# Performance work log

Hardware: AMD Instinct MI355X
Metric: run time of the kernel (lower is better)

## Reference

```python
import jax, jax.numpy as jnp
import numpy as np

N = 100000        # nodes
E = 1600000       # edges (avg degree 16)
IN = 128          # in_channels
HID = 256         # hidden_channels
OUT = 2           # out_channels
G = 512           # num graphs in batch


def setup_inputs() -> dict:
    key = jax.random.key(0)
    ks = jax.random.split(key, 10)
    x = jax.random.normal(ks[0], (N, IN), dtype=jnp.float32)
    edge_index = jax.random.randint(ks[1], (2, E), 0, N, dtype=jnp.int64)
    # sorted graph assignment, every graph non-empty (PyG-style batching)
    batch = (jnp.arange(N, dtype=jnp.int64) * G) // N
    s = 1.0 / np.sqrt(IN)
    sh = 1.0 / np.sqrt(2 * HID)
    sh1 = 1.0 / np.sqrt(HID)
    W_l = jax.random.uniform(ks[2], (HID, IN), jnp.float32, -s, s)   # SAGE lin_l (neighbors)
    b_l = jax.random.uniform(ks[3], (HID,), jnp.float32, -s, s)
    W_r = jax.random.uniform(ks[4], (HID, IN), jnp.float32, -s, s)   # SAGE lin_r (root), no bias
    W0 = jax.random.uniform(ks[5], (HID, IN), jnp.float32, -s, s)    # lin0
    b0 = jax.random.uniform(ks[5], (HID,), jnp.float32, -s, s)
    W1 = jax.random.uniform(ks[6], (HID, 2 * HID), jnp.float32, -sh, sh)  # lin1
    b1 = jax.random.uniform(ks[7], (HID,), jnp.float32, -sh, sh)
    W2 = jax.random.uniform(ks[8], (OUT, HID), jnp.float32, -sh1, sh1)    # lin2
    b2 = jax.random.uniform(ks[9], (OUT,), jnp.float32, -sh1, sh1)
    return {"x": x, "edge_index": edge_index, "batch": batch,
            "W_l": W_l, "b_l": b_l, "W_r": W_r,
            "W0": W0, "b0": b0, "W1": W1, "b1": b1, "W2": W2, "b2": b2}


def reference(x, edge_index, batch, W_l, b_l, W_r, W0, b0, W1, b1, W2, b2):
    src, dst = edge_index[0], edge_index[1]
    # SAGEConv: mean-aggregate neighbor features (gather -> scatter-add -> normalize)
    msg_sum = jax.ops.segment_sum(x[src], dst, num_segments=N)          # [N, IN]
    deg = jax.ops.segment_sum(jnp.ones((E,), x.dtype), dst, num_segments=N)
    aggr = msg_sum / jnp.maximum(deg, 1.0)[:, None]
    h = jax.nn.relu(aggr @ W_l.T + b_l + x @ W_r.T)                     # [N, HID]
    # global max pool per graph
    hp = jax.ops.segment_max(h, batch, num_segments=G)                  # [G, HID]
    # root node = first node of each graph (batch is sorted)
    root = jnp.searchsorted(batch, jnp.arange(G, dtype=batch.dtype))    # [G]
    news = jax.nn.relu(x[root] @ W0.T + b0)                             # [G, HID]
    h = jax.nn.relu(jnp.concatenate([news, hp], axis=-1) @ W1.T + b1)   # [G, HID]
    h = h @ W2.T + b2                                                   # [G, OUT]
    return jax.nn.log_softmax(h, axis=-1)
```

## Files before the change

kernel.cpp:

```cpp
#include <hip/hip_runtime.h>
#include <hip/hip_bf16.h>
#include <math.h>
#include <stdint.h>

#define IN_C 128
#define HID  256
#define OUT_C 2

#define BSHIFT 9
#define BNODES 512
#define EPB 4096

typedef __attribute__((ext_vector_type(8))) short short8;
typedef __attribute__((ext_vector_type(4))) float f32x4;
typedef __attribute__((ext_vector_type(2))) float f32x2;

#if defined(__has_builtin)
#if __has_builtin(__builtin_amdgcn_cvt_pk_f32_fp8) && __has_builtin(__builtin_amdgcn_cvt_pk_fp8_f32)
#define HAVE_FP8_CVT 1
#endif
#if __has_builtin(__builtin_amdgcn_global_load_lds)
#define HAVE_GLL 1
#endif
#endif

__device__ __forceinline__ ushort f2bf(float f) {
  uint32_t u = __float_as_uint(f);
  uint32_t r = u + 0x7FFF + ((u >> 16) & 1);
  return (ushort)(r >> 16);
}
__device__ __forceinline__ float bf2f(ushort b) {
  return __uint_as_float(((uint32_t)b) << 16);
}

#ifndef HAVE_FP8_CVT
__device__ __forceinline__ uint32_t f2fp8_1(float f) {
  uint32_t u = __float_as_uint(f);
  uint32_t s = (u >> 24) & 0x80;
  float a = fabsf(f);
  if (a >= 448.f) return s | 0x7E;
  if (a < 0.015625f) {
    uint32_t m = (uint32_t)(a * 512.f + 0.5f);
    return s | m;
  }
  uint32_t r = u & 0x7fffffff;
  r += 0x7FFFF + ((r >> 20) & 1);
  uint32_t e = (r >> 23) - 127;
  if ((int)e > 8) return s | 0x7E;
  return s | ((e + 7) << 3) | ((r >> 20) & 7);
}
__device__ __forceinline__ float fp8_2f(uint32_t b) {
  uint32_t s = (b & 0x80) << 24;
  uint32_t e = (b >> 3) & 0xF, m = b & 7;
  if (e == 0) { float f = (float)m * 0.001953125f; return s ? -f : f; }
  return __uint_as_float(s | ((e + 120) << 23) | (m << 20));
}
#endif

__device__ __forceinline__ void acc8f8(float* s, uint2 v) {
#ifdef HAVE_FP8_CVT
  f32x2 a = __builtin_amdgcn_cvt_pk_f32_fp8(v.x, false);
  f32x2 b = __builtin_amdgcn_cvt_pk_f32_fp8(v.x, true);
  f32x2 c = __builtin_amdgcn_cvt_pk_f32_fp8(v.y, false);
  f32x2 d = __builtin_amdgcn_cvt_pk_f32_fp8(v.y, true);
  s[0] += a.x; s[1] += a.y; s[2] += b.x; s[3] += b.y;
  s[4] += c.x; s[5] += c.y; s[6] += d.x; s[7] += d.y;
#else
  s[0] += fp8_2f(v.x & 0xff);        s[1] += fp8_2f((v.x >> 8) & 0xff);
  s[2] += fp8_2f((v.x >> 16) & 0xff); s[3] += fp8_2f(v.x >> 24);
  s[4] += fp8_2f(v.y & 0xff);        s[5] += fp8_2f((v.y >> 8) & 0xff);
  s[6] += fp8_2f((v.y >> 16) & 0xff); s[7] += fp8_2f(v.y >> 24);
#endif
}


__global__ void k_hist(const int* __restrict__ dst, int* __restrict__ bcount, int E) {
  __shared__ int h[256];
  int t = threadIdx.x;
  h[t] = 0;
  __syncthreads();
  for (int e = blockIdx.x * 256 + t; e < E; e += gridDim.x * 256)
    atomicAdd(&h[dst[e] >> BSHIFT], 1);
  __syncthreads();
  if (h[t]) atomicAdd(&bcount[t], h[t]);
}

__global__ void k_bucket_scan(const int* __restrict__ bcount,
                              int* __restrict__ bbase, int* __restrict__ bcursor) {
  __shared__ int sd[256];
  int t = threadIdx.x;
  int cnt = bcount[t];
  sd[t] = cnt;
  __syncthreads();
  for (int off = 1; off < 256; off <<= 1) {
    int v = (t >= off) ? sd[t - off] : 0;
    __syncthreads();
    sd[t] += v;
    __syncthreads();
  }
  int base = sd[t] - cnt;
  bbase[t] = base;
  bcursor[t] = base;
}

__global__ __launch_bounds__(256) void k_scatter(
    const int* __restrict__ src, const int* __restrict__ dst,
    int* __restrict__ bcursor, uint32_t* __restrict__ rec, int E) {
  __shared__ int h[256];
  __shared__ int bbase[256];
  __shared__ int lcur[256];
  int t = threadIdx.x;
  int e0 = blockIdx.x * EPB;
  int e1 = e0 + EPB < E ? e0 + EPB : E;
  h[t] = 0; lcur[t] = 0;
  __syncthreads();
  for (int e = e0 + t; e < e1; e += 256)
    atomicAdd(&h[dst[e] >> BSHIFT], 1);
  __syncthreads();
  if (h[t]) bbase[t] = atomicAdd(&bcursor[t], h[t]);
  __syncthreads();
  for (int e = e0 + t; e < e1; e += 256) {
    int d = dst[e];
    int b = d >> BSHIFT;
    int r = atomicAdd(&lcur[b], 1);
    rec[bbase[b] + r] = ((uint32_t)src[e] << BSHIFT) | ((uint32_t)d & (BNODES - 1));
  }
}

__global__ __launch_bounds__(256) void k_csr(
    const uint32_t* __restrict__ rec, const int* __restrict__ bbase,
    const int* __restrict__ bcount,
    int* __restrict__ row_start, int* __restrict__ deg,
    int* __restrict__ csr, int n) {
  __shared__ int ldeg[BNODES];
  __shared__ int lexcl[BNODES];
  __shared__ int ssum[256];
  int t = threadIdx.x;
  int b = blockIdx.x;
  int node0 = b << BSHIFT;
  int ebase = bbase[b];
  int ecnt = bcount[b];

  ldeg[t] = 0; ldeg[t + 256] = 0;
  __syncthreads();
  for (int i = t; i < ecnt; i += 256)
    atomicAdd(&ldeg[rec[ebase + i] & (BNODES - 1)], 1);
  __syncthreads();

  int v0 = ldeg[2 * t], v1 = ldeg[2 * t + 1];
  ssum[t] = v0 + v1;
  __syncthreads();
  for (int off = 1; off < 256; off <<= 1) {
    int v = (t >= off) ? ssum[t - off] : 0;
    __syncthreads();
    ssum[t] += v;
    __syncthreads();
  }
  int excl = ssum[t] - (v0 + v1);
  lexcl[2 * t] = excl;
  lexcl[2 * t + 1] = excl + v0;
  int node = node0 + 2 * t;
  if (node < n) { row_start[node] = ebase + excl; deg[node] = v0; }
  if (node + 1 < n) { row_start[node + 1] = ebase + excl + v0; deg[node + 1] = v1; }
  ldeg[2 * t] = 0; ldeg[2 * t + 1] = 0;
  __syncthreads();
  for (int i = t; i < ecnt; i += 256) {
    uint32_t r = rec[ebase + i];
    int li = r & (BNODES - 1);
    int k = atomicAdd(&ldeg[li], 1);
    csr[ebase + lexcl[li] + k] = (int)(r >> BSHIFT);
  }
}


__global__ void k_cast(const float* __restrict__ in, ushort* __restrict__ outb,
                       uint32_t* __restrict__ outf8, int n4) {
  int i = blockIdx.x * 256 + threadIdx.x;
  if (i < n4) {
    float4 v = ((const float4*)in)[i];
    ushort4 o;
    o.x = f2bf(v.x); o.y = f2bf(v.y); o.z = f2bf(v.z); o.w = f2bf(v.w);
    ((ushort4*)outb)[i] = o;
#ifdef HAVE_FP8_CVT
    int p = __builtin_amdgcn_cvt_pk_fp8_f32(v.x, v.y, 0, false);
    p = __builtin_amdgcn_cvt_pk_fp8_f32(v.z, v.w, p, true);
    outf8[i] = (uint32_t)p;
#else
    outf8[i] = f2fp8_1(v.x) | (f2fp8_1(v.y) << 8) | (f2fp8_1(v.z) << 16) |
               (f2fp8_1(v.w) << 24);
#endif
  }
}

__global__ void k_wcat(const float* __restrict__ Wl, const float* __restrict__ Wr,
                       ushort* __restrict__ Wcat) {
  int c = blockIdx.x, k = threadIdx.x;
  float v = (k < IN_C) ? Wl[(size_t)c * IN_C + k] : Wr[(size_t)c * IN_C + (k - IN_C)];
  Wcat[(size_t)c * (2 * IN_C) + k] = f2bf(v);
}

__global__ void k_cast2(const float* __restrict__ W0, const float* __restrict__ W1,
                        ushort* __restrict__ W0b, ushort* __restrict__ W1b) {
  const int N0 = HID * IN_C / 4;
  const int N1 = HID * 2 * HID / 4;
  int i = blockIdx.x * 256 + threadIdx.x;
  if (i < N0) {
    float4 v = ((const float4*)W0)[i];
    ushort4 o = {f2bf(v.x), f2bf(v.y), f2bf(v.z), f2bf(v.w)};
    ((ushort4*)W0b)[i] = o;
  } else if (i < N0 + N1) {
    int j = i - N0;
    float4 v = ((const float4*)W1)[j];
    ushort4 o = {f2bf(v.x), f2bf(v.y), f2bf(v.z), f2bf(v.w)};
    ((ushort4*)W1b)[j] = o;
  }
}


__global__ void k_aggr(const uint32_t* __restrict__ xf8, const int* __restrict__ csr,
                       const int* __restrict__ row_start, const int* __restrict__ deg,
                       ushort* __restrict__ aggr, int n) {
  int wid = threadIdx.x >> 6;
  int lane = threadIdx.x & 63;
  int node = blockIdx.x * 4 + wid;
  if (node >= n) return;
  int base = row_start[node];
  int d = deg[node];
  int q = lane >> 4, li = lane & 15;
  float s[8] = {};
  int i = q;
  for (; i + 12 < d; i += 16) {
    int n0 = csr[base + i];
    int n1 = csr[base + i + 4];
    int n2 = csr[base + i + 8];
    int n3 = csr[base + i + 12];
    uint2 a = ((const uint2*)(xf8 + (size_t)n0 * (IN_C / 4)))[li];
    uint2 b = ((const uint2*)(xf8 + (size_t)n1 * (IN_C / 4)))[li];
    uint2 c = ((const uint2*)(xf8 + (size_t)n2 * (IN_C / 4)))[li];
    uint2 e = ((const uint2*)(xf8 + (size_t)n3 * (IN_C / 4)))[li];
    acc8f8(s, a); acc8f8(s, b); acc8f8(s, c); acc8f8(s, e);
  }
  for (; i < d; i += 4) {
    int n0 = csr[base + i];
    uint2 a = ((const uint2*)(xf8 + (size_t)n0 * (IN_C / 4)))[li];
    acc8f8(s, a);
  }
#pragma unroll
  for (int j = 0; j < 8; ++j) {
    s[j] += __shfl_xor(s[j], 16);
    s[j] += __shfl_xor(s[j], 32);
  }
  if (q == 0) {
    float inv = 1.0f / (float)(d > 1 ? d : 1);
    uint4 o;
    o.x = (uint32_t)f2bf(s[0] * inv) | ((uint32_t)f2bf(s[1] * inv) << 16);
    o.y = (uint32_t)f2bf(s[2] * inv) | ((uint32_t)f2bf(s[3] * inv) << 16);
    o.z = (uint32_t)f2bf(s[4] * inv) | ((uint32_t)f2bf(s[5] * inv) << 16);
    o.w = (uint32_t)f2bf(s[6] * inv) | ((uint32_t)f2bf(s[7] * inv) << 16);
    ((uint4*)(aggr + (size_t)node * IN_C))[li] = o;
  }
}


#ifdef HAVE_GLL
__device__ __forceinline__ void load16_lds(const ushort* g, ushort* l) {
  __builtin_amdgcn_global_load_lds(
      (const __attribute__((address_space(1))) uint32_t*)g,
      (__attribute__((address_space(3))) uint32_t*)l, 16, 0, 0);
}
#endif

__global__ __launch_bounds__(256) void k_gemm_pool(
    const ushort* __restrict__ aggrb, const ushort* __restrict__ xb,
    const ushort* __restrict__ Wcat, const float* __restrict__ bl,
    const int* __restrict__ batch, float* __restrict__ hp, int n) {
  __shared__ ushort sA[2][64 * 32];
  __shared__ ushort sB[2][256 * 32];
  __shared__ float sbl[256];
  __shared__ int sBatch[64];

  int t = threadIdx.x;
  int n0 = blockIdx.x * 64;
  sbl[t] = bl[t];
  if (t < 64) sBatch[t] = (n0 + t < n) ? batch[n0 + t] : -1;

  int lane = t & 63, w = t >> 6;
  int q = lane >> 4, m = lane & 15;

  int rA = t >> 2, pA = t & 3;
  int cA = pA ^ ((rA >> 1) & 3);
  int gnA = n0 + rA; gnA = gnA < n ? gnA : n - 1;
  const ushort* baseAggr = aggrb + (size_t)gnA * IN_C + cA * 8;
  const ushort* baseX    = xb + (size_t)gnA * IN_C + cA * 8;
  int ldsA = rA * 32 + pA * 8;
  int pchunk = q ^ ((m >> 1) & 3);

  f32x4 acc[4][4] = {};

#ifdef HAVE_GLL
  auto stage = [&](int k0, int buf) {
    const ushort* srcA = (k0 < 4) ? baseAggr + k0 * 32 : baseX + (k0 - 4) * 32;
    load16_lds(srcA, &sA[buf][ldsA]);
#pragma unroll
    for (int it = 0; it < 4; ++it) {
      int rB = it * 64 + (t >> 2);
      int cB = (t & 3) ^ ((rB >> 1) & 3);
      load16_lds(Wcat + (size_t)rB * (2 * IN_C) + k0 * 32 + cB * 8,
                 &sB[buf][rB * 32 + (t & 3) * 8]);
    }
  };
  stage(0, 0);
  __syncthreads();
#pragma unroll
  for (int k0 = 0; k0 < 8; ++k0) {
    int cur = k0 & 1;
    if (k0 < 7) stage(k0 + 1, cur ^ 1);
    short8 af[4], bf[4];
#pragma unroll
    for (int rt = 0; rt < 4; ++rt)
      af[rt] = *(const short8*)&sA[cur][(rt * 16 + m) * 32 + pchunk * 8];
#pragma unroll
    for (int ct = 0; ct < 4; ++ct)
      bf[ct] = *(const short8*)&sB[cur][(w * 64 + ct * 16 + m) * 32 + pchunk * 8];
#pragma unroll
    for (int rt = 0; rt < 4; ++rt)
#pragma unroll
      for (int ct = 0; ct < 4; ++ct)
        acc[rt][ct] = __builtin_amdgcn_mfma_f32_16x16x32_bf16(af[rt], bf[ct], acc[rt][ct], 0, 0, 0);
    __syncthreads();
  }
#else
  for (int k0 = 0; k0 < 8; ++k0) {
    const ushort* srcA = (k0 < 4) ? baseAggr + k0 * 32 : baseX + (k0 - 4) * 32;
    uint4 vA = *(const uint4*)srcA;
    uint4 vB[4];
#pragma unroll
    for (int it = 0; it < 4; ++it) {
      int rB = it * 64 + (t >> 2);
      int cB = (t & 3) ^ ((rB >> 1) & 3);
      vB[it] = *(const uint4*)(Wcat + (size_t)rB * (2 * IN_C) + k0 * 32 + cB * 8);
    }
    __syncthreads();
    *(uint4*)&sA[0][ldsA] = vA;
#pragma unroll
    for (int it = 0; it < 4; ++it) {
      int rB = it * 64 + (t >> 2);
      *(uint4*)&sB[0][rB * 32 + (t & 3) * 8] = vB[it];
    }
    __syncthreads();
    short8 af[4], bf[4];
#pragma unroll
    for (int rt = 0; rt < 4; ++rt)
      af[rt] = *(const short8*)&sA[0][(rt * 16 + m) * 32 + pchunk * 8];
#pragma unroll
    for (int ct = 0; ct < 4; ++ct)
      bf[ct] = *(const short8*)&sB[0][(w * 64 + ct * 16 + m) * 32 + pchunk * 8];
#pragma unroll
    for (int rt = 0; rt < 4; ++rt)
#pragma unroll
      for (int ct = 0; ct < 4; ++ct)
        acc[rt][ct] = __builtin_amdgcn_mfma_f32_16x16x32_bf16(af[rt], bf[ct], acc[rt][ct], 0, 0, 0);
  }
#endif

  int last = n - 1 - n0; last = last < 63 ? last : 63;
  int gA = sBatch[0];
  int gB = sBatch[last];
#pragma unroll
  for (int ct = 0; ct < 4; ++ct) {
    int col = w * 64 + ct * 16 + m;
    float bias = sbl[col];
    float mA = 0.f, mB = 0.f;
#pragma unroll
    for (int rt = 0; rt < 4; ++rt) {
#pragma unroll
      for (int i = 0; i < 4; ++i) {
        int lr = rt * 16 + q * 4 + i;
        if (n0 + lr < n) {
          float v = fmaxf(acc[rt][ct][i] + bias, 0.f);
          if (sBatch[lr] == gA) mA = fmaxf(mA, v);
          else mB = fmaxf(mB, v);
        }
      }
    }
    mA = fmaxf(mA, __shfl_xor(mA, 16)); mA = fmaxf(mA, __shfl_xor(mA, 32));
    mB = fmaxf(mB, __shfl_xor(mB, 16)); mB = fmaxf(mB, __shfl_xor(mB, 32));
    if (q == 0) {
      atomicMax((int*)&hp[(size_t)gA * HID + col], __float_as_int(mA));
      if (gB != gA) atomicMax((int*)&hp[(size_t)gB * HID + col], __float_as_int(mB));
    }
  }
}


__global__ void k_root(const int* __restrict__ batch, int* __restrict__ root, int n) {
  int i = blockIdx.x * 256 + threadIdx.x;
  if (i < n) {
    int g = batch[i];
    if (i == 0 || batch[i - 1] != g) root[g] = i;
  }
}


__global__ __launch_bounds__(256) void k_tail(
    const ushort* __restrict__ xb, const float* __restrict__ hp,
    const int* __restrict__ root,
    const ushort* __restrict__ W0b, const float* __restrict__ b0,
    const ushort* __restrict__ W1b, const float* __restrict__ b1,
    const float* __restrict__ W2, const float* __restrict__ b2,
    float* __restrict__ out, int G) {
  __shared__ ushort sCat[64][264];
  __shared__ int sRoot[64];
  __shared__ float pp[256][2];

  int t = threadIdx.x;
  int g0 = blockIdx.x * 64;
  if (t < 64) sRoot[t] = (g0 + t < G) ? root[g0 + t] : 0;
  __syncthreads();

  int lane = t & 63, w = t >> 6;
  int q = lane >> 4, m = lane & 15;

  const ushort* xrow[4];
#pragma unroll
  for (int rt = 0; rt < 4; ++rt)
    xrow[rt] = xb + (size_t)sRoot[rt * 16 + m] * IN_C;

  {
    f32x4 acc[4][4] = {};
#pragma unroll
    for (int kc = 0; kc < 4; ++kc) {
      short8 af[4], bf[4];
#pragma unroll
      for (int rt = 0; rt < 4; ++rt)
        af[rt] = *(const short8*)(xrow[rt] + kc * 32 + q * 8);
#pragma unroll
      for (int ct = 0; ct < 4; ++ct) {
        int col = w * 64 + ct * 16 + m;
        bf[ct] = *(const short8*)(W0b + (size_t)col * IN_C + kc * 32 + q * 8);
      }
#pragma unroll
      for (int rt = 0; rt < 4; ++rt)
#pragma unroll
        for (int ct = 0; ct < 4; ++ct)
          acc[rt][ct] = __builtin_amdgcn_mfma_f32_16x16x32_bf16(af[rt], bf[ct], acc[rt][ct], 0, 0, 0);
    }
#pragma unroll
    for (int ct = 0; ct < 4; ++ct) {
      int col = w * 64 + ct * 16 + m;
      float bias = b0[col];
#pragma unroll
      for (int rt = 0; rt < 4; ++rt)
#pragma unroll
        for (int i = 0; i < 4; ++i) {
          int row = rt * 16 + q * 4 + i;
          sCat[row][col] = f2bf(fmaxf(acc[rt][ct][i] + bias, 0.f));
        }
    }
  }
  __syncthreads();

  f32x4 acc2[4][4] = {};
#pragma unroll
  for (int kc = 0; kc < 8; ++kc) {
    short8 af[4], bf[4];
#pragma unroll
    for (int rt = 0; rt < 4; ++rt)
      af[rt] = *(const short8*)&sCat[rt * 16 + m][kc * 32 + q * 8];
#pragma unroll
    for (int ct = 0; ct < 4; ++ct) {
      int col = w * 64 + ct * 16 + m;
      bf[ct] = *(const short8*)(W1b + (size_t)col * (2 * HID) + kc * 32 + q * 8);
    }
#pragma unroll
    for (int rt = 0; rt < 4; ++rt)
#pragma unroll
      for (int ct = 0; ct < 4; ++ct)
        acc2[rt][ct] = __builtin_amdgcn_mfma_f32_16x16x32_bf16(af[rt], bf[ct], acc2[rt][ct], 0, 0, 0);
  }
  __syncthreads();
#pragma unroll
  for (int it = 0; it < 16; ++it) {
    int idx = it * 256 + t;
    int r = idx >> 6, c4 = (idx & 63) * 4;
    if (g0 + r < G) {
      float4 v = *(const float4*)(hp + (size_t)(g0 + r) * HID + c4);
      ushort4 o = {f2bf(v.x), f2bf(v.y), f2bf(v.z), f2bf(v.w)};
      *(ushort4*)&sCat[r][c4] = o;
    }
  }
  __syncthreads();
#pragma unroll
  for (int kc = 8; kc < 16; ++kc) {
    short8 af[4], bf[4];
#pragma unroll
    for (int rt = 0; rt < 4; ++rt)
      af[rt] = *(const short8*)&sCat[rt * 16 + m][(kc - 8) * 32 + q * 8];
#pragma unroll
    for (int ct = 0; ct < 4; ++ct) {
      int col = w * 64 + ct * 16 + m;
      bf[ct] = *(const short8*)(W1b + (size_t)col * (2 * HID) + kc * 32 + q * 8);
    }
#pragma unroll
    for (int rt = 0; rt < 4; ++rt)
#pragma unroll
      for (int ct = 0; ct < 4; ++ct)
        acc2[rt][ct] = __builtin_amdgcn_mfma_f32_16x16x32_bf16(af[rt], bf[ct], acc2[rt][ct], 0, 0, 0);
  }
  __syncthreads();
#pragma unroll
  for (int ct = 0; ct < 4; ++ct) {
    int col = w * 64 + ct * 16 + m;
    float bias = b1[col];
#pragma unroll
    for (int rt = 0; rt < 4; ++rt)
#pragma unroll
      for (int i = 0; i < 4; ++i) {
        int row = rt * 16 + q * 4 + i;
        sCat[row][col] = f2bf(fmaxf(acc2[rt][ct][i] + bias, 0.f));
      }
  }
  __syncthreads();

  {
    int row = t >> 2, qq = t & 3;
    float p0 = 0.f, p1 = 0.f;
    for (int c = qq * 64; c < qq * 64 + 64; ++c) {
      float hv = bf2f(sCat[row][c]);
      p0 += hv * W2[c];
      p1 += hv * W2[HID + c];
    }
    pp[t][0] = p0; pp[t][1] = p1;
  }
  __syncthreads();
  if (t < 64 && g0 + t < G) {
    float l0 = b2[0], l1 = b2[1];
#pragma unroll
    for (int k = 0; k < 4; ++k) { l0 += pp[t * 4 + k][0]; l1 += pp[t * 4 + k][1]; }
    float mx = fmaxf(l0, l1);
    float ls = logf(expf(l0 - mx) + expf(l1 - mx));
    out[(size_t)(g0 + t) * 2 + 0] = l0 - mx - ls;
    out[(size_t)(g0 + t) * 2 + 1] = l1 - mx - ls;
  }
}


extern "C" void kernel_launch(void* const* d_in, const int* in_sizes, int n_in,
                              void* d_out, int out_size, void* d_ws, size_t ws_size,
                              hipStream_t stream) {
  const float* x  = (const float*)d_in[0];
  const int* ei   = (const int*)d_in[1];
  const int* batch= (const int*)d_in[2];
  const float* Wl = (const float*)d_in[3];
  const float* bl = (const float*)d_in[4];
  const float* Wr = (const float*)d_in[5];
  const float* W0 = (const float*)d_in[6];
  const float* b0 = (const float*)d_in[7];
  const float* W1 = (const float*)d_in[8];
  const float* b1 = (const float*)d_in[9];
  const float* W2 = (const float*)d_in[10];
  const float* b2 = (const float*)d_in[11];
  float* out = (float*)d_out;

  const int N = in_sizes[0] / IN_C;
  const int E = in_sizes[1] / 2;
  const int G = out_size / OUT_C;
  const int* src = ei;
  const int* dst = ei + E;
  const int NB = (N + BNODES - 1) >> BSHIFT;

  char* w = (char*)d_ws;
  int* deg       = (int*)w; w += (size_t)N * 4;
  int* row_start = (int*)w; w += (size_t)N * 4;
  int* bcount    = (int*)w; w += 1024;
  int* bbase     = (int*)w; w += 1024;
  int* bcursor   = (int*)w; w += 1024;
  int* root      = (int*)w; w += (size_t)G * 4;
  w = (char*)(((uintptr_t)w + 255) & ~(uintptr_t)255);
  int* csr       = (int*)w; w += (size_t)E * 4;
  w = (char*)(((uintptr_t)w + 255) & ~(uintptr_t)255);
  ushort* xb     = (ushort*)w; w += (size_t)N * IN_C * 2;
  uint32_t* xf8  = (uint32_t*)w; w += (size_t)N * IN_C;
  ushort* aggrb  = (ushort*)w; w += (size_t)N * IN_C * 2;
  ushort* Wcat   = (ushort*)w; w += (size_t)HID * (2 * IN_C) * 2;
  ushort* W0b    = (ushort*)w; w += (size_t)HID * IN_C * 2;
  ushort* W1b    = (ushort*)w; w += (size_t)HID * 2 * HID * 2;
  float* hp      = (float*)w; w += (size_t)G * HID * 4;
  uint32_t* rec  = (uint32_t*)aggrb;

  hipMemsetAsync(bcount, 0, 1024, stream);
  hipMemsetAsync(hp, 0, (size_t)G * HID * 4, stream);

  k_cast<<<((N * IN_C / 4) + 255) / 256, 256, 0, stream>>>(x, xb, xf8, N * IN_C / 4);
  k_wcat<<<HID, 2 * IN_C, 0, stream>>>(Wl, Wr, Wcat);
  k_cast2<<<(HID * IN_C / 4 + HID * 2 * HID / 4 + 255) / 256, 256, 0, stream>>>(W0, W1, W0b, W1b);
  k_hist<<<1024, 256, 0, stream>>>(dst, bcount, E);
  k_bucket_scan<<<1, 256, 0, stream>>>(bcount, bbase, bcursor);
  k_scatter<<<(E + EPB - 1) / EPB, 256, 0, stream>>>(src, dst, bcursor, rec, E);
  k_csr<<<NB, 256, 0, stream>>>(rec, bbase, bcount, row_start, deg, csr, N);
  k_root<<<(N + 255) / 256, 256, 0, stream>>>(batch, root, N);
  k_aggr<<<(N + 3) / 4, 256, 0, stream>>>(xf8, csr, row_start, deg, aggrb, N);
  k_gemm_pool<<<(N + 63) / 64, 256, 0, stream>>>(aggrb, xb, Wcat, bl, batch, hp, N);
  k_tail<<<(G + 63) / 64, 256, 0, stream>>>(xb, hp, root, W0b, b0, W1b, b1, W2, b2, out, G);
}
```

Before: 302.2 us.

## Fuse prep kernels, stage full A tile in LDS, stream weights from registers

Four small preprocessing kernels (x cast, weight concat/cast, W0/W1 cast, root finding) are merged into one launch to cut launch overhead. The GEMM+pool kernel now loads the whole 64x256 A tile into LDS once with an XOR swizzle and a single barrier, instead of double-buffering A and B in 32-wide k-chunks. Weight fragments are read straight from global memory (mostly L2-resident) into registers and prefetched one k-step ahead. The aggregation kernel switches to packed float2 accumulators. The trade-off is larger LDS per block (about 32 KB), which may lower occupancy, and more global traffic for the weight matrix.

Measured after the change: 299.9 us. About the same (-0.8%).

```diff
diff --git a/kernel.cpp b/kernel.cpp
--- a/kernel.cpp
+++ b/kernel.cpp
@@ -57,19 +57,17 @@
 }
 #endif
 
-__device__ __forceinline__ void acc8f8(float* s, uint2 v) {
+__device__ __forceinline__ void acc8f8v(f32x2* s, uint2 v) {
 #ifdef HAVE_FP8_CVT
-  f32x2 a = __builtin_amdgcn_cvt_pk_f32_fp8(v.x, false);
-  f32x2 b = __builtin_amdgcn_cvt_pk_f32_fp8(v.x, true);
-  f32x2 c = __builtin_amdgcn_cvt_pk_f32_fp8(v.y, false);
-  f32x2 d = __builtin_amdgcn_cvt_pk_f32_fp8(v.y, true);
-  s[0] += a.x; s[1] += a.y; s[2] += b.x; s[3] += b.y;
-  s[4] += c.x; s[5] += c.y; s[6] += d.x; s[7] += d.y;
+  s[0] += __builtin_amdgcn_cvt_pk_f32_fp8(v.x, false);
+  s[1] += __builtin_amdgcn_cvt_pk_f32_fp8(v.x, true);
+  s[2] += __builtin_amdgcn_cvt_pk_f32_fp8(v.y, false);
+  s[3] += __builtin_amdgcn_cvt_pk_f32_fp8(v.y, true);
 #else
-  s[0] += fp8_2f(v.x & 0xff);        s[1] += fp8_2f((v.x >> 8) & 0xff);
-  s[2] += fp8_2f((v.x >> 16) & 0xff); s[3] += fp8_2f(v.x >> 24);
-  s[4] += fp8_2f(v.y & 0xff);        s[5] += fp8_2f((v.y >> 8) & 0xff);
-  s[6] += fp8_2f((v.y >> 16) & 0xff); s[7] += fp8_2f(v.y >> 24);
+  s[0].x += fp8_2f(v.x & 0xff);         s[0].y += fp8_2f((v.x >> 8) & 0xff);
+  s[1].x += fp8_2f((v.x >> 16) & 0xff); s[1].y += fp8_2f(v.x >> 24);
+  s[2].x += fp8_2f(v.y & 0xff);         s[2].y += fp8_2f((v.y >> 8) & 0xff);
+  s[3].x += fp8_2f((v.y >> 16) & 0xff); s[3].y += fp8_2f(v.y >> 24);
 #endif
 }
 
@@ -173,46 +171,47 @@
 }
 
 
-__global__ void k_cast(const float* __restrict__ in, ushort* __restrict__ outb,
-                       uint32_t* __restrict__ outf8, int n4) {
+__global__ void k_prep(const float* __restrict__ x, ushort* __restrict__ xb,
+                       uint32_t* __restrict__ xf8, int n4,
+                       const float* __restrict__ Wl, const float* __restrict__ Wr,
+                       ushort* __restrict__ Wcat,
+                       const float* __restrict__ W0, ushort* __restrict__ W0b,
+                       const float* __restrict__ W1, ushort* __restrict__ W1b,
+                       const int* __restrict__ batch, int* __restrict__ root, int n) {
   int i = blockIdx.x * 256 + threadIdx.x;
   if (i < n4) {
-    float4 v = ((const float4*)in)[i];
-    ushort4 o;
-    o.x = f2bf(v.x); o.y = f2bf(v.y); o.z = f2bf(v.z); o.w = f2bf(v.w);
-    ((ushort4*)outb)[i] = o;
+    float4 v = ((const float4*)x)[i];
+    ushort4 o = {f2bf(v.x), f2bf(v.y), f2bf(v.z), f2bf(v.w)};
+    ((ushort4*)xb)[i] = o;
 #ifdef HAVE_FP8_CVT
     int p = __builtin_amdgcn_cvt_pk_fp8_f32(v.x, v.y, 0, false);
     p = __builtin_amdgcn_cvt_pk_fp8_f32(v.z, v.w, p, true);
-    outf8[i] = (uint32_t)p;
+    xf8[i] = (uint32_t)p;
 #else
-    outf8[i] = f2fp8_1(v.x) | (f2fp8_1(v.y) << 8) | (f2fp8_1(v.z) << 16) |
-               (f2fp8_1(v.w) << 24);
-#endif
-  }
-}
-
-__global__ void k_wcat(const float* __restrict__ Wl, const float* __restrict__ Wr,
-                       ushort* __restrict__ Wcat) {
-  int c = blockIdx.x, k = threadIdx.x;
-  float v = (k < IN_C) ? Wl[(size_t)c * IN_C + k] : Wr[(size_t)c * IN_C + (k - IN_C)];
-  Wcat[(size_t)c * (2 * IN_C) + k] = f2bf(v);
-}
-
-__global__ void k_cast2(const float* __restrict__ W0, const float* __restrict__ W1,
-                        ushort* __restrict__ W0b, ushort* __restrict__ W1b) {
-  const int N0 = HID * IN_C / 4;
-  const int N1 = HID * 2 * HID / 4;
-  int i = blockIdx.x * 256 + threadIdx.x;
-  if (i < N0) {
+    xf8[i] = f2fp8_1(v.x) | (f2fp8_1(v.y) << 8) | (f2fp8_1(v.z) << 16) |
+             (f2fp8_1(v.w) << 24);
+#endif
+  }
+  if (i < HID * (2 * IN_C) / 4) {
+    int c = i >> 6, c4 = (i & 63) * 4;
+    float4 v = (c4 < IN_C) ? *(const float4*)(Wl + (size_t)c * IN_C + c4)
+                           : *(const float4*)(Wr + (size_t)c * IN_C + (c4 - IN_C));
+    ushort4 o = {f2bf(v.x), f2bf(v.y), f2bf(v.z), f2bf(v.w)};
+    *(ushort4*)(Wcat + (size_t)c * (2 * IN_C) + c4) = o;
+  }
+  if (i < HID * IN_C / 4) {
     float4 v = ((const float4*)W0)[i];
     ushort4 o = {f2bf(v.x), f2bf(v.y), f2bf(v.z), f2bf(v.w)};
     ((ushort4*)W0b)[i] = o;
-  } else if (i < N0 + N1) {
-    int j = i - N0;
-    float4 v = ((const float4*)W1)[j];
+  }
+  if (i < HID * 2 * HID / 4) {
+    float4 v = ((const float4*)W1)[i];
     ushort4 o = {f2bf(v.x), f2bf(v.y), f2bf(v.z), f2bf(v.w)};
-    ((ushort4*)W1b)[j] = o;
+    ((ushort4*)W1b)[i] = o;
+  }
+  if (i < n) {
+    int g = batch[i];
+    if (i == 0 || batch[i - 1] != g) root[g] = i;
   }
 }
 
@@ -227,36 +226,37 @@
   int base = row_start[node];
   int d = deg[node];
   int q = lane >> 4, li = lane & 15;
-  float s[8] = {};
+  const uint2* xp = (const uint2*)xf8 + li;
+  f32x2 s[4] = {};
   int i = q;
   for (; i + 12 < d; i += 16) {
     int n0 = csr[base + i];
     int n1 = csr[base + i + 4];
     int n2 = csr[base + i + 8];
     int n3 = csr[base + i + 12];
-    uint2 a = ((const uint2*)(xf8 + (size_t)n0 * (IN_C / 4)))[li];
-    uint2 b = ((const uint2*)(xf8 + (size_t)n1 * (IN_C / 4)))[li];
-    uint2 c = ((const uint2*)(xf8 + (size_t)n2 * (IN_C / 4)))[li];
-    uint2 e = ((const uint2*)(xf8 + (size_t)n3 * (IN_C / 4)))[li];
-    acc8f8(s, a); acc8f8(s, b); acc8f8(s, c); acc8f8(s, e);
+    uint2 a = xp[(size_t)n0 * 16];
+    uint2 b = xp[(size_t)n1 * 16];
+    uint2 c = xp[(size_t)n2 * 16];
+    uint2 e = xp[(size_t)n3 * 16];
+    acc8f8v(s, a); acc8f8v(s, b); acc8f8v(s, c); acc8f8v(s, e);
   }
   for (; i < d; i += 4) {
     int n0 = csr[base + i];
-    uint2 a = ((const uint2*)(xf8 + (size_t)n0 * (IN_C / 4)))[li];
-    acc8f8(s, a);
-  }
-#pragma unroll
-  for (int j = 0; j < 8; ++j) {
-    s[j] += __shfl_xor(s[j], 16);
-    s[j] += __shfl_xor(s[j], 32);
+    uint2 a = xp[(size_t)n0 * 16];
+    acc8f8v(s, a);
+  }
+#pragma unroll
+  for (int j = 0; j < 4; ++j) {
+    s[j].x += __shfl_xor(s[j].x, 16); s[j].y += __shfl_xor(s[j].y, 16);
+    s[j].x += __shfl_xor(s[j].x, 32); s[j].y += __shfl_xor(s[j].y, 32);
   }
   if (q == 0) {
     float inv = 1.0f / (float)(d > 1 ? d : 1);
     uint4 o;
-    o.x = (uint32_t)f2bf(s[0] * inv) | ((uint32_t)f2bf(s[1] * inv) << 16);
-    o.y = (uint32_t)f2bf(s[2] * inv) | ((uint32_t)f2bf(s[3] * inv) << 16);
-    o.z = (uint32_t)f2bf(s[4] * inv) | ((uint32_t)f2bf(s[5] * inv) << 16);
-    o.w = (uint32_t)f2bf(s[6] * inv) | ((uint32_t)f2bf(s[7] * inv) << 16);
+    o.x = (uint32_t)f2bf(s[0].x * inv) | ((uint32_t)f2bf(s[0].y * inv) << 16);
+    o.y = (uint32_t)f2bf(s[1].x * inv) | ((uint32_t)f2bf(s[1].y * inv) << 16);
+    o.z = (uint32_t)f2bf(s[2].x * inv) | ((uint32_t)f2bf(s[2].y * inv) << 16);
+    o.w = (uint32_t)f2bf(s[3].x * inv) | ((uint32_t)f2bf(s[3].y * inv) << 16);
     ((uint4*)(aggr + (size_t)node * IN_C))[li] = o;
   }
 }
@@ -274,8 +274,7 @@
     const ushort* __restrict__ aggrb, const ushort* __restrict__ xb,
     const ushort* __restrict__ Wcat, const float* __restrict__ bl,
     const int* __restrict__ batch, float* __restrict__ hp, int n) {
-  __shared__ ushort sA[2][64 * 32];
-  __shared__ ushort sB[2][256 * 32];
+  __shared__ ushort sA[64 * 256];
   __shared__ float sbl[256];
   __shared__ int sBatch[64];
 
@@ -287,81 +286,53 @@
   int lane = t & 63, w = t >> 6;
   int q = lane >> 4, m = lane & 15;
 
-  int rA = t >> 2, pA = t & 3;
-  int cA = pA ^ ((rA >> 1) & 3);
-  int gnA = n0 + rA; gnA = gnA < n ? gnA : n - 1;
-  const ushort* baseAggr = aggrb + (size_t)gnA * IN_C + cA * 8;
-  const ushort* baseX    = xb + (size_t)gnA * IN_C + cA * 8;
-  int ldsA = rA * 32 + pA * 8;
-  int pchunk = q ^ ((m >> 1) & 3);
+#pragma unroll
+  for (int j = 0; j < 8; ++j) {
+    int s = (j * 4 + w) * 64 + lane;
+    int r = s >> 5, p = s & 31;
+    int c = p ^ (r & 15);
+    int gn = n0 + r; gn = gn < n ? gn : n - 1;
+    const ushort* g = (c < 16) ? aggrb + (size_t)gn * IN_C + c * 8
+                               : xb + (size_t)gn * IN_C + (c - 16) * 8;
+#ifdef HAVE_GLL
+    load16_lds(g, &sA[(size_t)s * 8]);
+#else
+    *(uint4*)&sA[(size_t)s * 8] = *(const uint4*)g;
+#endif
+  }
+
+  short8 bf_n[4];
+#pragma unroll
+  for (int ct = 0; ct < 4; ++ct)
+    bf_n[ct] = *(const short8*)(Wcat + (size_t)(w * 64 + ct * 16 + m) * (2 * IN_C) + q * 8);
+
+  __syncthreads();
 
   f32x4 acc[4][4] = {};
-
-#ifdef HAVE_GLL
-  auto stage = [&](int k0, int buf) {
-    const ushort* srcA = (k0 < 4) ? baseAggr + k0 * 32 : baseX + (k0 - 4) * 32;
-    load16_lds(srcA, &sA[buf][ldsA]);
-#pragma unroll
-    for (int it = 0; it < 4; ++it) {
-      int rB = it * 64 + (t >> 2);
-      int cB = (t & 3) ^ ((rB >> 1) & 3);
-      load16_lds(Wcat + (size_t)rB * (2 * IN_C) + k0 * 32 + cB * 8,
-                 &sB[buf][rB * 32 + (t & 3) * 8]);
-    }
-  };
-  stage(0, 0);
-  __syncthreads();
-#pragma unroll
-  for (int k0 = 0; k0 < 8; ++k0) {
-    int cur = k0 & 1;
-    if (k0 < 7) stage(k0 + 1, cur ^ 1);
-    short8 af[4], bf[4];
-#pragma unroll
-    for (int rt = 0; rt < 4; ++rt)
-      af[rt] = *(const short8*)&sA[cur][(rt * 16 + m) * 32 + pchunk * 8];
-#pragma unroll
-    for (int ct = 0; ct < 4; ++ct)
-      bf[ct] = *(const short8*)&sB[cur][(w * 64 + ct * 16 + m) * 32 + pchunk * 8];
+#pragma unroll
+  for (int kc = 0; kc < 8; ++kc) {
+    short8 bf[4];
+#pragma unroll
+    for (int ct = 0; ct < 4; ++ct) bf[ct] = bf_n[ct];
+    if (kc < 7) {
+#pragma unroll
+      for (int ct = 0; ct < 4; ++ct)
+        bf_n[ct] = *(const short8*)(Wcat + (size_t)(w * 64 + ct * 16 + m) * (2 * IN_C) +
+                                    (kc + 1) * 32 + q * 8);
+    }
+    short8 af[4];
+#pragma unroll
+    for (int rt = 0; rt < 4; ++rt) {
+      int r = rt * 16 + m;
+      int p = (kc * 4 + q) ^ m;
+      af[rt] = *(const short8*)&sA[r * 256 + p * 8];
+    }
 #pragma unroll
     for (int rt = 0; rt < 4; ++rt)
 #pragma unroll
       for (int ct = 0; ct < 4; ++ct)
         acc[rt][ct] = __builtin_amdgcn_mfma_f32_16x16x32_bf16(af[rt], bf[ct], acc[rt][ct], 0, 0, 0);
-    __syncthreads();
-  }
-#else
-  for (int k0 = 0; k0 < 8; ++k0) {
-    const ushort* srcA = (k0 < 4) ? baseAggr + k0 * 32 : baseX + (k0 - 4) * 32;
-    uint4 vA = *(const uint4*)srcA;
-    uint4 vB[4];
-#pragma unroll
-    for (int it = 0; it < 4; ++it) {
-      int rB = it * 64 + (t >> 2);
-      int cB = (t & 3) ^ ((rB >> 1) & 3);
-      vB[it] = *(const uint4*)(Wcat + (size_t)rB * (2 * IN_C) + k0 * 32 + cB * 8);
-    }
-    __syncthreads();
-    *(uint4*)&sA[0][ldsA] = vA;
-#pragma unroll
-    for (int it = 0; it < 4; ++it) {
-      int rB = it * 64 + (t >> 2);
-      *(uint4*)&sB[0][rB * 32 + (t & 3) * 8] = vB[it];
-    }
-    __syncthreads();
-    short8 af[4], bf[4];
-#pragma unroll
-    for (int rt = 0; rt < 4; ++rt)
-      af[rt] = *(const short8*)&sA[0][(rt * 16 + m) * 32 + pchunk * 8];
-#pragma unroll
-    for (int ct = 0; ct < 4; ++ct)
-      bf[ct] = *(const short8*)&sB[0][(w * 64 + ct * 16 + m) * 32 + pchunk * 8];
-#pragma unroll
-    for (int rt = 0; rt < 4; ++rt)
-#pragma unroll
-      for (int ct = 0; ct < 4; ++ct)
-        acc[rt][ct] = __builtin_amdgcn_mfma_f32_16x16x32_bf16(af[rt], bf[ct], acc[rt][ct], 0, 0, 0);
-  }
-#endif
+  }
 
   int last = n - 1 - n0; last = last < 63 ? last : 63;
   int gA = sBatch[0];
@@ -389,15 +360,6 @@
       atomicMax((int*)&hp[(size_t)gA * HID + col], __float_as_int(mA));
       if (gB != gA) atomicMax((int*)&hp[(size_t)gB * HID + col], __float_as_int(mB));
     }
-  }
-}
-
-
-__global__ void k_root(const int* __restrict__ batch, int* __restrict__ root, int n) {
-  int i = blockIdx.x * 256 + threadIdx.x;
-  if (i < n) {
-    int g = batch[i];
-    if (i == 0 || batch[i - 1] != g) root[g] = i;
   }
 }
 
@@ -591,14 +553,13 @@
   hipMemsetAsync(bcount, 0, 1024, stream);
   hipMemsetAsync(hp, 0, (size_t)G * HID * 4, stream);
 
-  k_cast<<<((N * IN_C / 4) + 255) / 256, 256, 0, stream>>>(x, xb, xf8, N * IN_C / 4);
-  k_wcat<<<HID, 2 * IN_C, 0, stream>>>(Wl, Wr, Wcat);
-  k_cast2<<<(HID * IN_C / 4 + HID * 2 * HID / 4 + 255) / 256, 256, 0, stream>>>(W0, W1, W0b, W1b);
+  int n4 = N * IN_C / 4;
+  k_prep<<<(n4 + 255) / 256, 256, 0, stream>>>(x, xb, xf8, n4, Wl, Wr, Wcat,
+                                               W0, W0b, W1, W1b, batch, root, N);
   k_hist<<<1024, 256, 0, stream>>>(dst, bcount, E);
   k_bucket_scan<<<1, 256, 0, stream>>>(bcount, bbase, bcursor);
   k_scatter<<<(E + EPB - 1) / EPB, 256, 0, stream>>>(src, dst, bcursor, rec, E);
   k_csr<<<NB, 256, 0, stream>>>(rec, bbase, bcount, row_start, deg, csr, N);
-  k_root<<<(N + 255) / 256, 256, 0, stream>>>(batch, root, N);
   k_aggr<<<(N + 3) / 4, 256, 0, stream>>>(xf8, csr, row_start, deg, aggrb, N);
   k_gemm_pool<<<(N + 63) / 64, 256, 0, stream>>>(aggrb, xb, Wcat, bl, batch, hp, N);
   k_tail<<<(G + 63) / 64, 256, 0, stream>>>(xb, hp, root, W0b, b0, W1b, b1, W2, b2, out, G);
```
